# Optimization experiments

Hardware: AMD Instinct MI355X
Metric: run time of the kernel (lower is better)

Reference implementation:

```python
import jax, jax.numpy as jnp
import numpy as np

EPS = 1e-12


def conv3(x, W, b):
    # x: [B,C,H,W], W: [O,I,3,3] -> SAME conv, stride 1
    y = jax.lax.conv_general_dilated(x, W, (1, 1), 'SAME',
                                     dimension_numbers=('NCHW', 'OIHW', 'NCHW'))
    return y + b[None, :, None, None]


def unfold3(x):
    # torch F.unfold(kernel=3, padding=1): [B,C,H,W] -> [B, C*9, H*W]
    B, C, H, W = x.shape
    xp = jnp.pad(x, ((0, 0), (0, 0), (1, 1), (1, 1)))
    patches = jnp.stack([xp[:, :, i:i + H, j:j + W]
                         for i in range(3) for j in range(3)], axis=2)  # [B,C,9,H,W]
    return patches.reshape(B, C * 9, H * W)


def fold3(u, H, W):
    # torch F.fold(kernel=3, padding=1): [B, C*9, H*W] -> [B,C,H,W] (overlap-add)
    B = u.shape[0]
    C = u.shape[1] // 9
    p = u.reshape(B, C, 3, 3, H, W)
    out = jnp.zeros((B, C, H + 2, W + 2), u.dtype)
    for i in range(3):
        for j in range(3):
            out = out.at[:, :, i:i + H, j:j + W].add(p[:, :, i, j])
    return out[:, :, 1:-1, 1:-1]


def l2norm(v, axis):
    n = jnp.sqrt(jnp.sum(v * v, axis=axis, keepdims=True))
    return v / jnp.maximum(n, EPS)


def setup_inputs() -> dict:
    key = jax.random.key(0)
    ks = jax.random.split(key, 10)
    in_c, q_c = 64, 32
    B, H, W = 1, 96, 96
    s = 0.05
    return {
        'x':  jax.random.normal(ks[0], (B, in_c, H, W), jnp.float32),
        'W1': jax.random.normal(ks[1], (in_c, in_c, 3, 3), jnp.float32) * s,
        'b1': jax.random.normal(ks[2], (in_c,), jnp.float32) * s,
        'W2': jax.random.normal(ks[3], (in_c, in_c, 3, 3), jnp.float32) * s,
        'b2': jax.random.normal(ks[4], (in_c,), jnp.float32) * s,
        'Wq': jax.random.normal(ks[5], (q_c, in_c, 3, 3), jnp.float32) * s,
        'bq': jax.random.normal(ks[6], (q_c,), jnp.float32) * s,
        'Wk': jax.random.normal(ks[7], (q_c, in_c, 3, 3), jnp.float32) * s,
        'bk': jax.random.normal(ks[8], (q_c,), jnp.float32) * s,
    }


def reference(x, W1, b1, W2, b2, Wq, bq, Wk, bk):
    TOPK = 5
    B, C, H, W = x.shape
    L = H * W

    feature = jax.nn.relu(conv3(jax.nn.relu(conv3(x, W1, b1)), W2, b2))
    q = conv3(x, Wq, bq)
    k = conv3(x, Wk, bk)

    q_unfold = l2norm(unfold3(q), axis=1)                      # [B, Q9, L]
    k_unfold = l2norm(jnp.swapaxes(unfold3(k), 1, 2), axis=2)  # [B, L, Q9]

    R_qk = jnp.einsum('blc,bcm->blm', k_unfold, q_unfold)      # [B, L_k, L_q]

    # topk over dim=1 (key positions) for each query position
    vals, idxs = jax.lax.top_k(jnp.swapaxes(R_qk, 1, 2), TOPK)  # [B, L_q, K]
    R_maxs = jnp.swapaxes(vals, 1, 2)                           # [B, K, L]
    R_indexs = jnp.swapaxes(idxs, 1, 2)                         # [B, K, L]

    x_unfold = unfold3(x)                                       # [B, C*9, L]
    acc = jnp.zeros_like(x)
    for i in range(1, TOPK):
        idx = R_indexs[:, i, :][:, None, :]                     # [B,1,L]
        T_unfold = jnp.take_along_axis(x_unfold, idx, axis=2)   # [B, C*9, L]
        T = fold3(T_unfold, H, W) / 9.0
        S = R_maxs[:, i, :].reshape(B, 1, H, W)
        acc = acc + T * S
    y = feature + x + acc / float(TOPK - 1)
    return y
```

## Files before the change

### kernel.cpp

```cpp
#include <hip/hip_runtime.h>
#include <math.h>

#define HH 96
#define WW 96
#define LL 9216
#define PW 98
#define PCH (PW * PW)
#define D9 288
#define TOPK 5
#define NK 6
#define NCAND 8
#define KSPLIT 32
#define CPQ (KSPLIT * NK)
#define KEYS_PER_SPLIT (LL / KSPLIT)
#define PASSES (KEYS_PER_SPLIT / 32)

typedef short short8 __attribute__((ext_vector_type(8)));
typedef float f32x16 __attribute__((ext_vector_type(16)));

__device__ __forceinline__ float  asf(unsigned u) { union { unsigned u; float f; } a; a.u = u; return a.f; }
__device__ __forceinline__ unsigned asu(float f)  { union { float f; unsigned u; } a; a.f = f; return a.u; }

__device__ __forceinline__ unsigned short f2bf(float f) {
    unsigned u = asu(f);
    unsigned r = u + 0x7fff + ((u >> 16) & 1);
    return (unsigned short)(r >> 16);
}

template<int N>
__device__ __forceinline__ void ins_med3(float* v, float x) {
    float nv[N];
    nv[0] = fmaxf(v[0], x);
    #pragma unroll
    for (int s = 1; s < N; ++s) nv[s] = __builtin_amdgcn_fmed3f(v[s-1], v[s], x);
    #pragma unroll
    for (int s = 0; s < N; ++s) v[s] = nv[s];
}

__device__ __forceinline__ bool better_tb(float av, int ai, float bv, int bi) {
    return (av > bv) || (av == bv && ai < bi);
}

template<int N>
__device__ __forceinline__ void insert_tb(float (&v)[N], int (&ix)[N], float nv, int ni) {
    if (better_tb(nv, ni, v[N-1], ix[N-1])) {
        v[N-1] = nv; ix[N-1] = ni;
        #pragma unroll
        for (int s = N-1; s > 0; --s) {
            if (better_tb(v[s], ix[s], v[s-1], ix[s-1])) {
                float tv = v[s]; v[s] = v[s-1]; v[s-1] = tv;
                int ti = ix[s]; ix[s] = ix[s-1]; ix[s-1] = ti;
            }
        }
    }
}

__global__ __launch_bounds__(256) void pad_init_kernel(
    const float* __restrict__ x, float* __restrict__ xpad, float* __restrict__ c1pad)
{
    int e = blockIdx.x * 256 + threadIdx.x;
    if (blockIdx.y == 1) { c1pad[e] = 0.0f; return; }
    int c = e / PCH, rem = e - c * PCH;
    int r = rem / PW, col = rem - r * PW;
    float val = 0.0f;
    if ((unsigned)(r - 1) < 96u && (unsigned)(col - 1) < 96u)
        val = x[(size_t)c * LL + (r - 1) * WW + (col - 1)];
    xpad[e] = val;
}

template<int NCO>
__device__ __forceinline__ void conv_pipe(
    const float* __restrict__ inpad, const float* __restrict__ Wt,
    const float* __restrict__ bias, int co0,
    float (&acc)[NCO][2])
{
    int t = blockIdx.x * 256 + threadIdx.x;
    int pix0 = t * 2;
    int y = pix0 / WW, x0 = pix0 - y * WW;
    const float* base = inpad + y * PW + x0;

    #pragma unroll
    for (int j = 0; j < NCO; ++j) acc[j][0] = acc[j][1] = bias[co0 + j];

    float2 A[3][2], B[3][2];
    #pragma unroll
    for (int u = 0; u < 3; ++u) {
        A[u][0] = *(const float2*)(base + u * PW);
        A[u][1] = *(const float2*)(base + u * PW + 2);
    }

    #pragma unroll 1
    for (int ci = 0; ci < 64; ci += 2) {
        const float* nb = base + (size_t)(ci + 1) * PCH;
        #pragma unroll
        for (int u = 0; u < 3; ++u) {
            B[u][0] = *(const float2*)(nb + u * PW);
            B[u][1] = *(const float2*)(nb + u * PW + 2);
        }
        {
            const float* wb = Wt + ((size_t)co0 * 64 + ci) * 9;
            #pragma unroll
            for (int j = 0; j < NCO; ++j) {
                const float* wp = wb + (size_t)j * 64 * 9;
                #pragma unroll
                for (int u = 0; u < 3; ++u) {
                    float r0 = A[u][0].x, r1 = A[u][0].y, r2 = A[u][1].x, r3 = A[u][1].y;
                    float w0 = wp[u*3], w1 = wp[u*3+1], w2 = wp[u*3+2];
                    acc[j][0] = fmaf(r0, w0, acc[j][0]);
                    acc[j][1] = fmaf(r1, w0, acc[j][1]);
                    acc[j][0] = fmaf(r1, w1, acc[j][0]);
                    acc[j][1] = fmaf(r2, w1, acc[j][1]);
                    acc[j][0] = fmaf(r2, w2, acc[j][0]);
                    acc[j][1] = fmaf(r3, w2, acc[j][1]);
                }
            }
        }
        if (ci + 2 < 64) {
            const float* nb2 = base + (size_t)(ci + 2) * PCH;
            #pragma unroll
            for (int u = 0; u < 3; ++u) {
                A[u][0] = *(const float2*)(nb2 + u * PW);
                A[u][1] = *(const float2*)(nb2 + u * PW + 2);
            }
        }
        {
            const float* wb = Wt + ((size_t)co0 * 64 + (ci + 1)) * 9;
            #pragma unroll
            for (int j = 0; j < NCO; ++j) {
                const float* wp = wb + (size_t)j * 64 * 9;
                #pragma unroll
                for (int u = 0; u < 3; ++u) {
                    float r0 = B[u][0].x, r1 = B[u][0].y, r2 = B[u][1].x, r3 = B[u][1].y;
                    float w0 = wp[u*3], w1 = wp[u*3+1], w2 = wp[u*3+2];
                    acc[j][0] = fmaf(r0, w0, acc[j][0]);
                    acc[j][1] = fmaf(r1, w0, acc[j][1]);
                    acc[j][0] = fmaf(r1, w1, acc[j][0]);
                    acc[j][1] = fmaf(r2, w1, acc[j][1]);
                    acc[j][0] = fmaf(r2, w2, acc[j][0]);
                    acc[j][1] = fmaf(r3, w2, acc[j][1]);
                }
            }
        }
    }
}

__global__ __launch_bounds__(256) void conv_stage1_kernel(
    const float* __restrict__ xpad,
    const float* __restrict__ W1, const float* __restrict__ b1, float* __restrict__ c1pad,
    const float* __restrict__ Wq, const float* __restrict__ bq,
    const float* __restrict__ Wk, const float* __restrict__ bk,
    float* __restrict__ qq, float* __restrict__ kk)
{
    int g = blockIdx.y;
    int pix0 = (blockIdx.x * 256 + threadIdx.x) * 2;
    int y = pix0 / WW, x0 = pix0 - y * WW;

    if (g < 16) {
        float acc[4][2];
        conv_pipe<4>(xpad, W1, b1, g * 4, acc);
        #pragma unroll
        for (int j = 0; j < 4; ++j) {
            float* o = c1pad + (size_t)(g * 4 + j) * PCH + (y + 1) * PW + (x0 + 1);
            o[0] = fmaxf(acc[j][0], 0.0f);
            o[1] = fmaxf(acc[j][1], 0.0f);
        }
    } else if (g < 24) {
        float acc[4][2];
        conv_pipe<4>(xpad, Wq, bq, (g - 16) * 4, acc);
        #pragma unroll
        for (int j = 0; j < 4; ++j)
            *(float2*)(qq + (size_t)((g - 16) * 4 + j) * LL + pix0) = make_float2(acc[j][0], acc[j][1]);
    } else {
        float acc[4][2];
        conv_pipe<4>(xpad, Wk, bk, (g - 24) * 4, acc);
        #pragma unroll
        for (int j = 0; j < 4; ++j)
            *(float2*)(kk + (size_t)((g - 24) * 4 + j) * LL + pix0) = make_float2(acc[j][0], acc[j][1]);
    }
}

__global__ __launch_bounds__(256) void conv2_kernel(
    const float* __restrict__ c1pad, const float* __restrict__ W2,
    const float* __restrict__ b2, float* __restrict__ feat)
{
    int pix0 = (blockIdx.x * 256 + threadIdx.x) * 2;
    float acc[2][2];
    conv_pipe<2>(c1pad, W2, b2, blockIdx.y * 2, acc);
    #pragma unroll
    for (int j = 0; j < 2; ++j) {
        float2 o;
        o.x = fmaxf(acc[j][0], 0.0f);
        o.y = fmaxf(acc[j][1], 0.0f);
        *(float2*)(feat + (size_t)(blockIdx.y * 2 + j) * LL + pix0) = o;
    }
}

__global__ __launch_bounds__(256) void transpose_x_kernel(
    const float* __restrict__ x, float* __restrict__ xT)
{
    __shared__ float t[64][65];
    int pix0 = blockIdx.x * 64;
    int lp = threadIdx.x & 63, cg = threadIdx.x >> 6;
    #pragma unroll
    for (int cc = 0; cc < 16; ++cc) {
        int c = cg * 16 + cc;
        t[c][lp] = x[(size_t)c * LL + pix0 + lp];
    }
    __syncthreads();
    #pragma unroll
    for (int pp = 0; pp < 16; ++pp) {
        int pl = cg * 16 + pp;
        xT[(size_t)(pix0 + pl) * 64 + lp] = t[lp][pl];
    }
}

__global__ __launch_bounds__(256) void unfold_norm_kernel(
    const float* __restrict__ qq, float* __restrict__ q_f32, unsigned short* __restrict__ q_bf,
    const float* __restrict__ kk, float* __restrict__ k_f32, unsigned short* __restrict__ k_bf)
{
    const float* in; float* o32; unsigned short* obf;
    if (blockIdx.y == 0) { in = qq; o32 = q_f32; obf = q_bf; }
    else                 { in = kk; o32 = k_f32; obf = k_bf; }

    __shared__ float tile[3][32][34];
    __shared__ float inv_s[32];
    int tid = threadIdx.x;
    int l0 = blockIdx.x * 32;
    int y = l0 / WW, xb = l0 % WW;

    #pragma unroll
    for (int j = 0; j < 13; ++j) {
        int f = j * 256 + tid;
        if (f < 3 * 32 * 34) {
            int col = f % 34, cc = (f / 34) & 31, r = f / (34 * 32);
            int yy = y + r - 1, xv = xb + col - 1;
            float val = ((unsigned)yy < 96u && (unsigned)xv < 96u)
                        ? in[(size_t)cc * LL + yy * 96 + xv] : 0.0f;
            tile[r][cc][col] = val;
        }
    }
    __syncthreads();

    {
        int pxl = tid >> 3, sub = tid & 7;
        float ss = 0.0f;
        #pragma unroll
        for (int cc = 0; cc < 4; ++cc) {
            int c = sub * 4 + cc;
            #pragma unroll
            for (int u = 0; u < 3; ++u)
                #pragma unroll
                for (int v = 0; v < 3; ++v) {
                    float val = tile[u][c][pxl + v];
                    ss = fmaf(val, val, ss);
                }
        }
        ss += __shfl_xor(ss, 1);
        ss += __shfl_xor(ss, 2);
        ss += __shfl_xor(ss, 4);
        if (sub == 0) inv_s[pxl] = 1.0f / fmaxf(sqrtf(ss), 1e-12f);
    }
    __syncthreads();

    #pragma unroll 1
    for (int it = 0; it < 9; ++it) {
        int e = it * 256 + tid;
        int pxl = e / 72, dc = e - pxl * 72;
        int l = l0 + pxl;
        float inv = inv_s[pxl];
        float4 o; float* op = &o.x;
        #pragma unroll
        for (int i = 0; i < 4; ++i) {
            int d = dc * 4 + i;
            int c = d / 9, rm = d - c * 9;
            int u = rm / 3, v = rm - u * 3;
            op[i] = tile[u][c][pxl + v] * inv;
        }
        *(float4*)(o32 + (size_t)l * D9 + dc * 4) = o;
        unsigned short b4[4];
        #pragma unroll
        for (int i = 0; i < 4; ++i) b4[i] = f2bf(op[i]);
        *(uint2*)(obf + (size_t)l * D9 + dc * 4) = *(uint2*)b4;
    }
}

__global__ __launch_bounds__(256) void repack_afrag_kernel(
    const unsigned short* __restrict__ kn_bf, short8* __restrict__ kn_afrag)
{
    int flat = blockIdx.x * 256 + threadIdx.x;
    int lane = flat & 63;
    int g = flat >> 6;
    int dg = g % 18;
    int sp = g / 18;
    int key = sp * 32 + (lane & 31);
    int d0 = dg * 16 + (lane >> 5) * 8;
    kn_afrag[flat] = *(const short8*)(kn_bf + (size_t)key * D9 + d0);
}

__global__ __launch_bounds__(256, 2) void topk_mfma_kernel(
    const unsigned short* __restrict__ qn_bf, const short8* __restrict__ kn_afrag,
    float* __restrict__ valsQ)
{
    int tid  = threadIdx.x;
    int lane = tid & 63;
    int col = lane & 31, khalf = lane >> 5;
    int qtile = blockIdx.x >> 5;
    int split = blockIdx.x & 31;
    int q0w = qtile * 256 + (tid >> 6) * 64;
    int key0 = split * KEYS_PER_SPLIT;

    short8 qf[2][18];
    #pragma unroll
    for (int b = 0; b < 2; ++b) {
        const unsigned short* qrow = qn_bf + (size_t)(q0w + b*32 + col) * D9 + khalf * 8;
        #pragma unroll
        for (int dg = 0; dg < 18; ++dg)
            qf[b][dg] = *(const short8*)(qrow + dg * 16);
    }

    float lv0[NK], lv1[NK];
    #pragma unroll
    for (int s = 0; s < NK; ++s) { lv0[s] = -INFINITY; lv1[s] = -INFINITY; }

    const short8* ka = kn_afrag + (size_t)split * (PASSES * 18 * 64) + lane;

    #pragma unroll 1
    for (int p = 0; p < PASSES; ++p) {
        const short8* kp = ka + p * (18 * 64);
        f32x16 acc0 = {}, acc1 = {};
        #pragma unroll
        for (int dg = 0; dg < 18; ++dg) {
            short8 af = kp[dg * 64];
            acc0 = __builtin_amdgcn_mfma_f32_32x32x16_bf16(af, qf[0][dg], acc0, 0, 0, 0);
            acc1 = __builtin_amdgcn_mfma_f32_32x32x16_bf16(af, qf[1][dg], acc1, 0, 0, 0);
        }

        int lbase = p * 32 + 4 * khalf;
        #pragma unroll
        for (int r = 0; r < 16; ++r) {
            unsigned lkey = (unsigned)(lbase + (r & 3) + 8 * (r >> 2));
            ins_med3<NK>(lv0, asf((asu(acc0[r]) & 0xFFFFFE00u) | lkey));
            ins_med3<NK>(lv1, asf((asu(acc1[r]) & 0xFFFFFE00u) | lkey));
        }
    }

    #pragma unroll
    for (int b = 0; b < 2; ++b) {
        float* lv = b ? lv1 : lv0;
        float pv[NK];
        #pragma unroll
        for (int s = 0; s < NK; ++s) pv[s] = __shfl_xor(lv[s], 32);
        #pragma unroll
        for (int s = 0; s < NK; ++s) ins_med3<NK>(lv, pv[s]);
        if (lane < 32) {
            int q = q0w + b * 32 + col;
            float* vq = valsQ + (size_t)q * CPQ + split * NK;
            #pragma unroll
            for (int s = 0; s < NK; ++s) vq[s] = lv[s];
        }
    }
    (void)key0;
}

__global__ __launch_bounds__(256) void rerank_kernel(
    const float* __restrict__ valsQ,
    const float* __restrict__ qn_f32, const float* __restrict__ kn_f32,
    float* __restrict__ vals, int* __restrict__ idxs)
{
    int tid = threadIdx.x;
    int lane = tid & 63;
    int half = lane >> 5, l32 = lane & 31;
    int q = blockIdx.x * 8 + (tid >> 6) * 2 + half;

    const float* vq = valsQ + (size_t)q * CPQ + l32 * NK;
    float v[NK];
    #pragma unroll
    for (int s = 0; s < NK; ++s) v[s] = vq[s];

    int ckey[NCAND];
    #pragma unroll
    for (int it = 0; it < NCAND; ++it) {
        float cv = v[0];
        int cl = l32;
        #pragma unroll
        for (int st = 1; st < 32; st <<= 1) {
            float ov = __shfl_xor(cv, st);
            int ol = __shfl_xor(cl, st);
            if (ov > cv || (ov == cv && ol < cl)) { cv = ov; cl = ol; }
        }
        ckey[it] = cl * KEYS_PER_SPLIT + (int)(asu(cv) & 0x1FFu);
        if (cl == l32) {
            #pragma unroll
            for (int s = 0; s < NK-1; ++s) v[s] = v[s+1];
            v[NK-1] = -INFINITY;
        }
    }

    int r = l32 >> 2, part = l32 & 3;
    const float4* qr = (const float4*)(qn_f32 + (size_t)q * D9) + part * 18;
    const float4* kr = (const float4*)(kn_f32 + (size_t)ckey[r] * D9) + part * 18;
    float s0 = 0.f, s1 = 0.f, s2 = 0.f, s3 = 0.f;
    #pragma unroll
    for (int i2 = 0; i2 < 18; ++i2) {
        float4 a = qr[i2], b = kr[i2];
        s0 = fmaf(a.x, b.x, s0); s1 = fmaf(a.y, b.y, s1);
        s2 = fmaf(a.z, b.z, s2); s3 = fmaf(a.w, b.w, s3);
    }
    float sc = (s0 + s1) + (s2 + s3);
    sc += __shfl_xor(sc, 1);
    sc += __shfl_xor(sc, 2);

    float bv[TOPK]; int bi[TOPK];
    #pragma unroll
    for (int s = 0; s < TOPK; ++s) { bv[s] = -INFINITY; bi[s] = 0x7fffffff; }
    #pragma unroll
    for (int cc = 0; cc < NCAND; ++cc) {
        float sv = __shfl(sc, half * 32 + cc * 4);
        insert_tb<TOPK>(bv, bi, sv, ckey[cc]);
    }
    if (l32 == 0) {
        #pragma unroll
        for (int s = 0; s < TOPK; ++s) {
            vals[(size_t)s * LL + q] = bv[s];
            idxs[(size_t)s * LL + q] = bi[s];
        }
    }
}

__global__ __launch_bounds__(256) void gather_out_kernel(
    const float* __restrict__ xT, const float* __restrict__ feat,
    const float* __restrict__ vals, const int* __restrict__ idxs,
    float* __restrict__ out)
{
    int wave = threadIdx.x >> 6, lane = threadIdx.x & 63;
    int pix = blockIdx.x * 4 + wave;
    int y = pix / WW, x0 = pix - y * WW;
    float acc = 0.0f;
    #pragma unroll 1
    for (int s = 1; s < TOPK; ++s) {
        float S = vals[(size_t)s * LL + pix] * (1.0f/9.0f);
        #pragma unroll
        for (int i = 0; i < 3; ++i) {
            int qy = y + 1 - i;
            #pragma unroll
            for (int j = 0; j < 3; ++j) {
                int qx = x0 + 1 - j;
                if ((unsigned)qy < 96u && (unsigned)qx < 96u) {
                    int l = idxs[(size_t)s * LL + qy * WW + qx];
                    int yl = l / WW, xl = l - yl * WW;
                    int sy = yl + i - 1, sx = xl + j - 1;
                    if ((unsigned)sy < 96u && (unsigned)sx < 96u)
                        acc = fmaf(S, xT[(size_t)(sy * WW + sx) * 64 + lane], acc);
                }
            }
        }
    }
    out[(size_t)lane * LL + pix] = feat[(size_t)lane * LL + pix]
                                 + xT[(size_t)pix * 64 + lane] + acc * 0.25f;
}

extern "C" void kernel_launch(void* const* d_in, const int* in_sizes, int n_in,
                              void* d_out, int out_size, void* d_ws, size_t ws_size,
                              hipStream_t stream)
{
    (void)in_sizes; (void)n_in; (void)out_size; (void)ws_size;
    const float* x  = (const float*)d_in[0];
    const float* W1 = (const float*)d_in[1];
    const float* b1 = (const float*)d_in[2];
    const float* W2 = (const float*)d_in[3];
    const float* b2 = (const float*)d_in[4];
    const float* Wq = (const float*)d_in[5];
    const float* bq = (const float*)d_in[6];
    const float* Wk = (const float*)d_in[7];
    const float* bk = (const float*)d_in[8];
    float* out = (float*)d_out;

    char* p = (char*)d_ws;
    float* xpad   = (float*)p;            p += (size_t)64 * PCH * 4;
    float* c1pad  = (float*)p;            p += (size_t)64 * PCH * 4;
    float* feat   = (float*)p;            p += (size_t)64 * LL * 4;
    float* xT     = (float*)p;            p += (size_t)64 * LL * 4;
    float* qq     = (float*)p;            p += (size_t)32 * LL * 4;
    float* kk     = (float*)p;            p += (size_t)32 * LL * 4;
    float* qn_f32 = (float*)p;            p += (size_t)LL * D9 * 4;
    float* kn_f32 = (float*)p;            p += (size_t)LL * D9 * 4;
    unsigned short* qn_bf = (unsigned short*)p;  p += (size_t)LL * D9 * 2;
    unsigned short* kn_bf = (unsigned short*)p;  p += (size_t)LL * D9 * 2;
    short8* kn_afrag = (short8*)p;        p += (size_t)KSPLIT * PASSES * 18 * 64 * 16;
    float* valsQ  = (float*)p;            p += (size_t)LL * CPQ * 4;
    float* vals   = (float*)p;            p += (size_t)TOPK * LL * 4;
    int*   idxs   = (int*)p;              p += (size_t)TOPK * LL * 4;

    pad_init_kernel<<<dim3(2401, 2), 256, 0, stream>>>(x, xpad, c1pad);
    conv_stage1_kernel<<<dim3(18, 32), 256, 0, stream>>>(xpad, W1, b1, c1pad, Wq, bq, Wk, bk, qq, kk);
    unfold_norm_kernel<<<dim3(288, 2), 256, 0, stream>>>(qq, qn_f32, qn_bf, kk, kn_f32, kn_bf);
    repack_afrag_kernel<<<1296, 256, 0, stream>>>(kn_bf, kn_afrag);
    topk_mfma_kernel<<<36 * KSPLIT, 256, 0, stream>>>(qn_bf, kn_afrag, valsQ);
    conv2_kernel<<<dim3(18, 32), 256, 0, stream>>>(c1pad, W2, b2, feat);
    transpose_x_kernel<<<144, 256, 0, stream>>>(x, xT);
    rerank_kernel<<<LL / 8, 256, 0, stream>>>(valsQ, qn_f32, kn_f32, vals, idxs);
    gather_out_kernel<<<LL / 4, 256, 0, stream>>>(xT, feat, vals, idxs, out);
}
```

Measured before the change: 326.3 us.

## Software-pipeline key fragment loads and halve per-wave query tiles in topk MFMA kernel

Each wave in the top-k MFMA kernel now handles 32 queries instead of 64, and the grid doubles to 72*32 blocks. Blocks are ordered split-major so neighbouring blocks share the same key split. Key A-fragments are double-buffered in registers (cur/nxt), so the next pass's loads are in flight while the current pass's MFMAs and top-k inserts run. In exchange, each key fragment is loaded twice as often across the grid and each pass has less MFMA work to hide latency behind, while the two 18-fragment buffers raise register pressure.

```diff
diff --git a/kernel.cpp b/kernel.cpp
--- a/kernel.cpp
+++ b/kernel.cpp
@@ -304,62 +304,91 @@
     int tid  = threadIdx.x;
     int lane = tid & 63;
     int col = lane & 31, khalf = lane >> 5;
-    int qtile = blockIdx.x >> 5;
-    int split = blockIdx.x & 31;
-    int q0w = qtile * 256 + (tid >> 6) * 64;
-    int key0 = split * KEYS_PER_SPLIT;
-
-    short8 qf[2][18];
-    #pragma unroll
-    for (int b = 0; b < 2; ++b) {
-        const unsigned short* qrow = qn_bf + (size_t)(q0w + b*32 + col) * D9 + khalf * 8;
+    int split = blockIdx.x / 72;
+    int qtile = blockIdx.x - split * 72;
+    int q0w = qtile * 128 + (tid >> 6) * 32;
+
+    short8 qf[18];
+    {
+        const unsigned short* qrow = qn_bf + (size_t)(q0w + col) * D9 + khalf * 8;
         #pragma unroll
         for (int dg = 0; dg < 18; ++dg)
-            qf[b][dg] = *(const short8*)(qrow + dg * 16);
-    }
-
-    float lv0[NK], lv1[NK];
-    #pragma unroll
-    for (int s = 0; s < NK; ++s) { lv0[s] = -INFINITY; lv1[s] = -INFINITY; }
+            qf[dg] = *(const short8*)(qrow + dg * 16);
+    }
+
+    float lv[NK];
+    #pragma unroll
+    for (int s = 0; s < NK; ++s) lv[s] = -INFINITY;
 
     const short8* ka = kn_afrag + (size_t)split * (PASSES * 18 * 64) + lane;
 
+    short8 cur[18], nxt[18];
+    #pragma unroll
+    for (int dg = 0; dg < 18; ++dg) cur[dg] = ka[dg * 64];
+
     #pragma unroll 1
-    for (int p = 0; p < PASSES; ++p) {
-        const short8* kp = ka + p * (18 * 64);
-        f32x16 acc0 = {}, acc1 = {};
-        #pragma unroll
-        for (int dg = 0; dg < 18; ++dg) {
-            short8 af = kp[dg * 64];
-            acc0 = __builtin_amdgcn_mfma_f32_32x32x16_bf16(af, qf[0][dg], acc0, 0, 0, 0);
-            acc1 = __builtin_amdgcn_mfma_f32_32x32x16_bf16(af, qf[1][dg], acc1, 0, 0, 0);
-        }
-
-        int lbase = p * 32 + 4 * khalf;
+    for (int p = 0; p < PASSES - 1; p += 2) {
+        {
+            const short8* k1 = ka + (size_t)(p + 1) * (18 * 64);
+            #pragma unroll
+            for (int dg = 0; dg < 18; ++dg) nxt[dg] = k1[dg * 64];
+        }
+        {
+            f32x16 acc = {};
+            #pragma unroll
+            for (int dg = 0; dg < 18; ++dg)
+                acc = __builtin_amdgcn_mfma_f32_32x32x16_bf16(cur[dg], qf[dg], acc, 0, 0, 0);
+            int lbase = p * 32 + 4 * khalf;
+            #pragma unroll
+            for (int r = 0; r < 16; ++r) {
+                unsigned lkey = (unsigned)(lbase + (r & 3) + 8 * (r >> 2));
+                ins_med3<NK>(lv, asf((asu(acc[r]) & 0xFFFFFE00u) | lkey));
+            }
+        }
+        if (p + 2 < PASSES) {
+            const short8* k2 = ka + (size_t)(p + 2) * (18 * 64);
+            #pragma unroll
+            for (int dg = 0; dg < 18; ++dg) cur[dg] = k2[dg * 64];
+        }
+        {
+            f32x16 acc = {};
+            #pragma unroll
+            for (int dg = 0; dg < 18; ++dg)
+                acc = __builtin_amdgcn_mfma_f32_32x32x16_bf16(nxt[dg], qf[dg], acc, 0, 0, 0);
+            int lbase = (p + 1) * 32 + 4 * khalf;
+            #pragma unroll
+            for (int r = 0; r < 16; ++r) {
+                unsigned lkey = (unsigned)(lbase + (r & 3) + 8 * (r >> 2));
+                ins_med3<NK>(lv, asf((asu(acc[r]) & 0xFFFFFE00u) | lkey));
+            }
+        }
+    }
+    {
+        f32x16 acc = {};
+        #pragma unroll
+        for (int dg = 0; dg < 18; ++dg)
+            acc = __builtin_amdgcn_mfma_f32_32x32x16_bf16(cur[dg], qf[dg], acc, 0, 0, 0);
+        int lbase = (PASSES - 1) * 32 + 4 * khalf;
         #pragma unroll
         for (int r = 0; r < 16; ++r) {
             unsigned lkey = (unsigned)(lbase + (r & 3) + 8 * (r >> 2));
-            ins_med3<NK>(lv0, asf((asu(acc0[r]) & 0xFFFFFE00u) | lkey));
-            ins_med3<NK>(lv1, asf((asu(acc1[r]) & 0xFFFFFE00u) | lkey));
-        }
-    }
-
-    #pragma unroll
-    for (int b = 0; b < 2; ++b) {
-        float* lv = b ? lv1 : lv0;
+            ins_med3<NK>(lv, asf((asu(acc[r]) & 0xFFFFFE00u) | lkey));
+        }
+    }
+
+    {
         float pv[NK];
         #pragma unroll
         for (int s = 0; s < NK; ++s) pv[s] = __shfl_xor(lv[s], 32);
         #pragma unroll
         for (int s = 0; s < NK; ++s) ins_med3<NK>(lv, pv[s]);
         if (lane < 32) {
-            int q = q0w + b * 32 + col;
+            int q = q0w + col;
             float* vq = valsQ + (size_t)q * CPQ + split * NK;
             #pragma unroll
             for (int s = 0; s < NK; ++s) vq[s] = lv[s];
         }
     }
-    (void)key0;
 }
 
 __global__ __launch_bounds__(256) void rerank_kernel(
@@ -495,7 +524,7 @@
     conv_stage1_kernel<<<dim3(18, 32), 256, 0, stream>>>(xpad, W1, b1, c1pad, Wq, bq, Wk, bk, qq, kk);
     unfold_norm_kernel<<<dim3(288, 2), 256, 0, stream>>>(qq, qn_f32, qn_bf, kk, kn_f32, kn_bf);
     repack_afrag_kernel<<<1296, 256, 0, stream>>>(kn_bf, kn_afrag);
-    topk_mfma_kernel<<<36 * KSPLIT, 256, 0, stream>>>(qn_bf, kn_afrag, valsQ);
+    topk_mfma_kernel<<<72 * KSPLIT, 256, 0, stream>>>(qn_bf, kn_afrag, valsQ);
     conv2_kernel<<<dim3(18, 32), 256, 0, stream>>>(c1pad, W2, b2, feat);
     transpose_x_kernel<<<144, 256, 0, stream>>>(x, xT);
     rerank_kernel<<<LL / 8, 256, 0, stream>>>(valsQ, qn_f32, kn_f32, vals, idxs);
```

Result: faster. 300.1 us (-8.0%).
